# Performance work log

Measured on AMD Instinct MI355X. Metric: run time of the kernel, lower is better.

The kernel has to match this reference:

```python
import jax, jax.numpy as jnp
import numpy as np

# model constants (match init_kwargs)
VOCAB = 32000
DIM = 1024
HEADS = 8
DH = DIM // HEADS
LAYERS = 2
K_SLOTS = 128
KR = 16   # read top-k
KW = 16   # write top-k
CHUNK = 256
GAMMA = 0.9  # slot memory decay per chunk


def setup_inputs() -> dict:
    key = jax.random.key(0)
    ks = jax.random.split(key, 12)
    B, S = 2, 4096
    s = 0.02
    inp = {
        "tokens": jax.random.randint(ks[0], (B, S), 0, VOCAB, dtype=jnp.int32),
        "embed": jax.random.normal(ks[1], (VOCAB, DIM), jnp.float32) * s,
        "Wq": jax.random.normal(ks[2], (LAYERS, DIM, DIM), jnp.float32) * s,
        "Wk": jax.random.normal(ks[3], (LAYERS, DIM, DIM), jnp.float32) * s,
        "Wv": jax.random.normal(ks[4], (LAYERS, DIM, DIM), jnp.float32) * s,
        "Wo": jax.random.normal(ks[5], (LAYERS, DIM, DIM), jnp.float32) * s,
        "slot_keys": jax.random.normal(ks[6], (LAYERS, HEADS, K_SLOTS, DH), jnp.float32) * s,
        "ln_g": jnp.ones((LAYERS, DIM), jnp.float32),
        "ln_b": jnp.zeros((LAYERS, DIM), jnp.float32),
        "fg": jnp.ones((DIM,), jnp.float32),
        "fb": jnp.zeros((DIM,), jnp.float32),
        "Wout": jax.random.normal(ks[7], (DIM, VOCAB), jnp.float32) * s,
        "bout": jnp.zeros((VOCAB,), jnp.float32),
    }
    return inp


def _layer_norm(x, g, b, eps=1e-5):
    mu = jnp.mean(x, axis=-1, keepdims=True)
    var = jnp.var(x, axis=-1, keepdims=True)
    return (x - mu) * jax.lax.rsqrt(var + eps) * g + b


def _mhdsra2_layer(x, M, Wq, Wk, Wv, Wo, sk, causal_mask):
    # x: [B,T,D], M: [B,H,K,dh] slot value memory, sk: [H,K,dh] slot keys
    B, T, D = x.shape
    H, K, dh = sk.shape
    scale = 1.0 / np.sqrt(dh)
    q = (x @ Wq).reshape(B, T, H, dh).transpose(0, 2, 1, 3)  # bhtd
    k = (x @ Wk).reshape(B, T, H, dh).transpose(0, 2, 1, 3)
    v = (x @ Wv).reshape(B, T, H, dh).transpose(0, 2, 1, 3)
    # --- slot READ: top-kr addressed gather from memory ---
    rs = jnp.einsum('bhtd,hkd->bhtk', q, sk) * scale           # [B,H,T,K]
    rv, ri = jax.lax.top_k(rs, KR)                              # [B,H,T,KR]
    rw = jax.nn.softmax(rv, axis=-1)
    gathered = jnp.take_along_axis(M[:, :, None, :, :], ri[..., None], axis=3)  # [B,H,T,KR,dh]
    read = jnp.einsum('bhtk,bhtkd->bhtd', rw, gathered)
    # --- local causal attention within chunk (local_window = chunk_size) ---
    att = jnp.einsum('bhtd,bhsd->bhts', q, k) * scale
    att = jnp.where(causal_mask, att, jnp.float32(-1e9))
    att = jax.nn.softmax(att, axis=-1)
    local = jnp.einsum('bhts,bhsd->bhtd', att, v)
    out = (local + read).transpose(0, 2, 1, 3).reshape(B, T, D) @ Wo
    # --- slot WRITE: top-kw addressed scatter into memory ---
    ws = jnp.einsum('bhtd,hkd->bhtk', k, sk) * scale
    wv_, wi = jax.lax.top_k(ws, KW)
    ww = jax.nn.softmax(wv_, axis=-1)                           # [B,H,T,KW]
    contrib = ww[..., None] * v[:, :, :, None, :]               # [B,H,T,KW,dh]
    bI = jnp.arange(B)[:, None, None, None]
    hI = jnp.arange(H)[None, :, None, None]
    delta = jnp.zeros_like(M).at[bI, hI, wi].add(contrib)
    M_next = GAMMA * M + delta
    return out, M_next


def reference(tokens, embed, Wq, Wk, Wv, Wo, slot_keys, ln_g, ln_b, fg, fb, Wout, bout):
    B, S = tokens.shape
    hidden = embed[tokens]                                      # [B,S,D]
    n_chunks = S // CHUNK
    chunks = hidden.reshape(B, n_chunks, CHUNK, DIM).transpose(1, 0, 2, 3)
    M0 = jnp.zeros((LAYERS, B, HEADS, K_SLOTS, DH), jnp.float32)
    causal_mask = jnp.tril(jnp.ones((CHUNK, CHUNK), bool))

    def body(M_all, chunk):
        new_Ms = []
        for l in range(LAYERS):
            residual = chunk
            xn = _layer_norm(chunk, ln_g[l], ln_b[l])
            out, Mn = _mhdsra2_layer(xn, M_all[l], Wq[l], Wk[l], Wv[l], Wo[l], slot_keys[l], causal_mask)
            new_Ms.append(jax.lax.stop_gradient(Mn))  # detach_state=True
            chunk = residual + out
        return jnp.stack(new_Ms), chunk

    _, outs = jax.lax.scan(body, M0, chunks)                    # [n_chunks,B,T,D]
    out = outs.transpose(1, 0, 2, 3).reshape(B, S, DIM)
    out = _layer_norm(out, fg, fb)
    return out @ Wout + bout                                     # [B,S,VOCAB]
```

## Files before the change

kernel.cpp:

```cpp
#include <hip/hip_runtime.h>

#define DIMM 1024
#define NHEADS 8
#define DH 128
#define NSLOTS 128
#define CHUNK 256
#define NCHUNK 16
#define NB 2
#define SEQ 4096
#define NROWS (NB * SEQ)
#define NVOCAB 32000
#define GAMMA64 0.9
#define SCALE64 0.08838834764831845
#define TAU 1e-6f
#define MAXFLAG 65536

typedef unsigned short u16;
typedef __attribute__((ext_vector_type(4))) float f32x4;
typedef __attribute__((ext_vector_type(8))) short s16x8;

struct alignas(8) u16x4 { u16 x, y, z, w; };

__device__ __forceinline__ u16 f2bf(float f) {
  union { float f; unsigned u; } v; v.f = f;
  return (u16)((v.u + 0x7FFFu + ((v.u >> 16) & 1u)) >> 16);
}
__device__ __forceinline__ float bf2f(u16 u) {
  union { unsigned u; float f; } v; v.u = ((unsigned)u) << 16; return v.f;
}
__device__ __forceinline__ void split3s(float x, u16& h, u16& m, u16& l) {
  h = f2bf(x); float r = x - bf2f(h);
  m = f2bf(r); float r2 = r - bf2f(m);
  l = f2bf(r2);
}

__device__ __forceinline__ void gld16(void* lds, const void* g) {
  __builtin_amdgcn_global_load_lds(
      (const __attribute__((address_space(1))) unsigned*)g,
      (__attribute__((address_space(3))) unsigned*)lds, 16, 0, 0);
}
__device__ __forceinline__ f32x4 mfma16(s16x8 a, s16x8 b, f32x4 c) {
  return __builtin_amdgcn_mfma_f32_16x16x32_bf16(a, b, c, 0, 0, 0);
}

__global__ __launch_bounds__(256) void embed64_kernel(
    const int* __restrict__ tok, const float* __restrict__ emb,
    double* __restrict__ hid) {
  const int row = blockIdx.x;
  const int t = tok[row];
  const float4 v = ((const float4*)(emb + (size_t)t * DIMM))[threadIdx.x];
  double* o = hid + (size_t)row * DIMM + threadIdx.x * 4;
  o[0] = (double)v.x; o[1] = (double)v.y; o[2] = (double)v.z; o[3] = (double)v.w;
}

template <int MODE>
__global__ __launch_bounds__(256) void ln64_kernel(
    const double* __restrict__ x, const float* __restrict__ g,
    const float* __restrict__ bb, double* __restrict__ o64,
    u16* __restrict__ oh, u16* __restrict__ om, u16* __restrict__ ol) {
  const int row = blockIdx.x, tid = threadIdx.x;
  const double* xr = x + (size_t)row * DIMM + tid * 4;
  const double v0 = xr[0], v1 = xr[1], v2 = xr[2], v3 = xr[3];
  __shared__ double red[4];
  double s1 = v0 + v1 + v2 + v3;
#pragma unroll
  for (int off = 32; off >= 1; off >>= 1) s1 += __shfl_xor(s1, off);
  if ((tid & 63) == 0) red[tid >> 6] = s1;
  __syncthreads();
  const double mu = (red[0] + red[1] + red[2] + red[3]) * (1.0 / DIMM);
  __syncthreads();
  const double d0 = v0 - mu, d1 = v1 - mu, d2 = v2 - mu, d3 = v3 - mu;
  double s2 = d0 * d0 + d1 * d1 + d2 * d2 + d3 * d3;
#pragma unroll
  for (int off = 32; off >= 1; off >>= 1) s2 += __shfl_xor(s2, off);
  if ((tid & 63) == 0) red[tid >> 6] = s2;
  __syncthreads();
  const double var = (red[0] + red[1] + red[2] + red[3]) * (1.0 / DIMM);
  const double rs = 1.0 / sqrt(var + 1e-5);
  const float4 g4 = ((const float4*)g)[tid];
  const float4 b4 = ((const float4*)bb)[tid];
  const double y0 = d0 * rs * (double)g4.x + (double)b4.x;
  const double y1 = d1 * rs * (double)g4.y + (double)b4.y;
  const double y2 = d2 * rs * (double)g4.z + (double)b4.z;
  const double y3 = d3 * rs * (double)g4.w + (double)b4.w;
  if (MODE == 0) {
    double* o = o64 + (size_t)row * DIMM + tid * 4;
    o[0] = y0; o[1] = y1; o[2] = y2; o[3] = y3;
    u16x4 rh, rm, rl;
    split3s((float)y0, rh.x, rm.x, rl.x);
    split3s((float)y1, rh.y, rm.y, rl.y);
    split3s((float)y2, rh.z, rm.z, rl.z);
    split3s((float)y3, rh.w, rm.w, rl.w);
    ((u16x4*)(oh + (size_t)row * DIMM))[tid] = rh;
    ((u16x4*)(om + (size_t)row * DIMM))[tid] = rm;
    ((u16x4*)(ol + (size_t)row * DIMM))[tid] = rl;
  } else {
    u16x4 r;
    r.x = f2bf((float)y0); r.y = f2bf((float)y1);
    r.z = f2bf((float)y2); r.w = f2bf((float)y3);
    ((u16x4*)(oh + (size_t)row * DIMM))[tid] = r;
  }
}

__global__ void transconv3_kernel(const float* __restrict__ W,
                                  u16* __restrict__ WTh, u16* __restrict__ WTm,
                                  u16* __restrict__ WTl, int K, int N) {
  __shared__ float tile[32][33];
  const int n0 = blockIdx.x * 32, k0 = blockIdx.y * 32;
  const int tx = threadIdx.x, ty = threadIdx.y;
#pragma unroll
  for (int i = 0; i < 4; i++)
    tile[ty + 8 * i][tx] = W[(size_t)(k0 + ty + 8 * i) * N + n0 + tx];
  __syncthreads();
#pragma unroll
  for (int i = 0; i < 4; i++) {
    u16 h, m, l;
    split3s(tile[tx][ty + 8 * i], h, m, l);
    const size_t o = (size_t)(n0 + ty + 8 * i) * K + k0 + tx;
    WTh[o] = h; WTm[o] = m; WTl[o] = l;
  }
}

__global__ __launch_bounds__(256) void cvt3_32_kernel(
    const float* __restrict__ in, u16* __restrict__ oh, u16* __restrict__ om,
    u16* __restrict__ ol) {
  const size_t i = (size_t)blockIdx.x * 256 + threadIdx.x;
  const float4 v = ((const float4*)in)[i];
  u16x4 rh, rm, rl;
  split3s(v.x, rh.x, rm.x, rl.x); split3s(v.y, rh.y, rm.y, rl.y);
  split3s(v.z, rh.z, rm.z, rl.z); split3s(v.w, rh.w, rm.w, rl.w);
  ((u16x4*)oh)[i] = rh; ((u16x4*)om)[i] = rm; ((u16x4*)ol)[i] = rl;
}

__global__ __launch_bounds__(256) void w2_kernel(const float* __restrict__ W,
                                                 const float* __restrict__ sk,
                                                 double* __restrict__ W2) {
  __shared__ float sksh[128];
  const int r = blockIdx.x, h = r >> 7;
  const int tid = threadIdx.x;
  if (tid < 128) sksh[tid] = sk[(size_t)r * DH + tid];
  __syncthreads();
  for (int d = tid; d < DIMM; d += 256) {
    const float* wrow = W + (size_t)d * DIMM + h * DH;
    double acc = 0.0;
#pragma unroll 8
    for (int j = 0; j < 128; j++) acc += (double)wrow[j] * (double)sksh[j];
    W2[(size_t)r * DIMM + d] = acc;
  }
}

template <bool RES, typename TC>
__global__ __launch_bounds__(256) void gemm3d_kernel(
    const u16* __restrict__ Ah, const u16* __restrict__ Am,
    const u16* __restrict__ Al, const u16* __restrict__ Bh,
    const u16* __restrict__ Bm, const u16* __restrict__ Bl,
    TC* __restrict__ C, const TC* __restrict__ Cres, int M, int N, int K) {
  __shared__ u16 lds[6 * 128 * 32];
  const int tid = threadIdx.x;
  const int bn = blockIdx.x, bm = blockIdx.y;
  const int wid = tid >> 6, lane = tid & 63;
  const int wr = (wid >> 1) * 64, wc = (wid & 1) * 64;
  f32x4 acc[4][4] = {};
  const int row0 = tid >> 2;
  const int colb = (tid & 3) << 4;
  const u16* Gs[6] = {Ah, Am, Al, Bh, Bm, Bl};
  const char* g0[6];
  const char* g1[6];
  char* lb[6];
#pragma unroll
  for (int i = 0; i < 6; i++) {
    const int rbase = (i < 3 ? bm : bn) * 128;
    g0[i] = (const char*)Gs[i] + ((size_t)(rbase + row0) * K) * 2 + colb;
    g1[i] = (const char*)Gs[i] + ((size_t)(rbase + row0 + 64) * K) * 2 + colb;
    lb[i] = (char*)lds + i * 8192 + (tid & 192) * 16;
  }
  const int fo = (lane & 15) * 64 + (lane >> 4) * 16;
  const char* paH = (const char*)lds + 0 + wr * 64 + fo;
  const char* paM = paH + 8192;
  const char* paL = paH + 16384;
  const char* pbH = (const char*)lds + 24576 + wc * 64 + fo;
  const char* pbM = pbH + 8192;
  const char* pbL = pbH + 16384;

  for (int k0 = 0; k0 < K; k0 += 32) {
    const size_t kb = (size_t)k0 * 2;
#pragma unroll
    for (int i = 0; i < 6; i++) {
      gld16(lb[i], g0[i] + kb);
      gld16(lb[i] + 4096, g1[i] + kb);
    }
    __syncthreads();
    s16x8 bh[4], bm_[4], bl[4];
#pragma unroll
    for (int n = 0; n < 4; n++) {
      bh[n] = *(const s16x8*)(pbH + n * 1024);
      bm_[n] = *(const s16x8*)(pbM + n * 1024);
      bl[n] = *(const s16x8*)(pbL + n * 1024);
    }
#pragma unroll
    for (int m = 0; m < 4; m++) {
      const s16x8 ah = *(const s16x8*)(paH + m * 1024);
      const s16x8 am = *(const s16x8*)(paM + m * 1024);
      const s16x8 al = *(const s16x8*)(paL + m * 1024);
#pragma unroll
      for (int n = 0; n < 4; n++) {
        f32x4 t = acc[m][n];
        t = mfma16(al, bh[n], t);
        t = mfma16(ah, bl[n], t);
        t = mfma16(am, bm_[n], t);
        t = mfma16(am, bh[n], t);
        t = mfma16(ah, bm_[n], t);
        t = mfma16(ah, bh[n], t);
        acc[m][n] = t;
      }
    }
    __syncthreads();
  }
#pragma unroll
  for (int m = 0; m < 4; m++)
#pragma unroll
    for (int n = 0; n < 4; n++)
#pragma unroll
      for (int j = 0; j < 4; j++) {
        const int r = bm * 128 + wr + m * 16 + (lane >> 4) * 4 + j;
        const int c = bn * 128 + wc + n * 16 + (lane & 15);
        TC v = (TC)acc[m][n][j];
        if (RES) v += Cres[(size_t)r * N + c];
        C[(size_t)r * N + c] = v;
      }
}

__global__ __launch_bounds__(256) void score3_kernel(
    const u16* __restrict__ Qh, const u16* __restrict__ Qm,
    const u16* __restrict__ Ql, const u16* __restrict__ Kh3,
    const u16* __restrict__ Km3, const u16* __restrict__ Kl3,
    const u16* __restrict__ skh, const u16* __restrict__ skm,
    const u16* __restrict__ skl, float* __restrict__ S) {
  __shared__ u16 lds[6 * 128 * 32];
  const int tid = threadIdx.x;
  const int bm = blockIdx.x;
  const int y = blockIdx.y;
  const int which = y >> 4, b = (y >> 3) & 1, h = y & 7;
  const u16* Ah = which ? Kh3 : Qh;
  const u16* Am = which ? Km3 : Qm;
  const u16* Al = which ? Kl3 : Ql;
  const int wid = tid >> 6, lane = tid & 63;
  const int wr = (wid >> 1) * 64, wc = (wid & 1) * 64;
  f32x4 acc[4][4] = {};
  const int row0 = tid >> 2;
  const int colb = (tid & 3) << 4;
  const size_t arow = (size_t)(b * SEQ + bm * 128);
  const u16* Gs[6] = {Ah, Am, Al, skh, skm, skl};
  const char* g0[6];
  const char* g1[6];
  char* lb[6];
#pragma unroll
  for (int i = 0; i < 6; i++) {
    if (i < 3) {
      g0[i] = (const char*)Gs[i] + (arow + row0) * 2048 + h * 256 + colb;
      g1[i] = (const char*)Gs[i] + (arow + row0 + 64) * 2048 + h * 256 + colb;
    } else {
      g0[i] = (const char*)Gs[i] + ((size_t)h * 128 + row0) * 256 + colb;
      g1[i] = (const char*)Gs[i] + ((size_t)h * 128 + row0 + 64) * 256 + colb;
    }
    lb[i] = (char*)lds + i * 8192 + (tid & 192) * 16;
  }
  const int fo = (lane & 15) * 64 + (lane >> 4) * 16;
  const char* paH = (const char*)lds + 0 + wr * 64 + fo;
  const char* paM = paH + 8192;
  const char* paL = paH + 16384;
  const char* pbH = (const char*)lds + 24576 + wc * 64 + fo;
  const char* pbM = pbH + 8192;
  const char* pbL = pbH + 16384;

  for (int k0 = 0; k0 < DH; k0 += 32) {
    const size_t kb = (size_t)k0 * 2;
#pragma unroll
    for (int i = 0; i < 6; i++) {
      gld16(lb[i], g0[i] + kb);
      gld16(lb[i] + 4096, g1[i] + kb);
    }
    __syncthreads();
    s16x8 bh[4], bm_[4], bl[4];
#pragma unroll
    for (int n = 0; n < 4; n++) {
      bh[n] = *(const s16x8*)(pbH + n * 1024);
      bm_[n] = *(const s16x8*)(pbM + n * 1024);
      bl[n] = *(const s16x8*)(pbL + n * 1024);
    }
#pragma unroll
    for (int m = 0; m < 4; m++) {
      const s16x8 ah = *(const s16x8*)(paH + m * 1024);
      const s16x8 am = *(const s16x8*)(paM + m * 1024);
      const s16x8 al = *(const s16x8*)(paL + m * 1024);
#pragma unroll
      for (int n = 0; n < 4; n++) {
        f32x4 t = acc[m][n];
        t = mfma16(al, bh[n], t);
        t = mfma16(ah, bl[n], t);
        t = mfma16(am, bm_[n], t);
        t = mfma16(am, bh[n], t);
        t = mfma16(ah, bm_[n], t);
        t = mfma16(ah, bh[n], t);
        acc[m][n] = t;
      }
    }
    __syncthreads();
  }
  const size_t sbase =
      (size_t)which * 65536 + (size_t)(b * 8 + h) * 4096 + (size_t)bm * 128;
#pragma unroll
  for (int m = 0; m < 4; m++)
#pragma unroll
    for (int n = 0; n < 4; n++)
#pragma unroll
      for (int j = 0; j < 4; j++) {
        const int r = wr + m * 16 + (lane >> 4) * 4 + j;
        const int c = wc + n * 16 + (lane & 15);
        S[(sbase + r) * NSLOTS + c] = acc[m][n][j];
      }
}

__global__ __launch_bounds__(256) void select_kernel(
    const float* __restrict__ S, int* __restrict__ riQ, int* __restrict__ riK,
    double* __restrict__ rwQ, double* __restrict__ rwK,
    int* __restrict__ fcnts, int* __restrict__ flq, int* __restrict__ flk) {
  const int which = blockIdx.y;
  int* oidx = which ? riK : riQ;
  double* ow = which ? rwK : rwQ;
  int* fcnt = fcnts + which;
  int* flist = which ? flk : flq;
  const int wid = threadIdx.x >> 6, lane = threadIdx.x & 63;
  const int rid = blockIdx.x * 4 + wid;
  const float2 sv =
      *(const float2*)(S + ((size_t)which * 65536 + rid) * NSLOTS + lane * 2);
  const float sc = (float)SCALE64;
  float v0 = sv.x * sc, v1 = sv.y * sc;
  const int i0 = lane * 2, i1 = lane * 2 + 1;
  float selv = -1e30f; int seli = 0;
  for (int it = 0; it < 17; it++) {
    float m; int mi;
    if (v1 > v0) { m = v1; mi = i1; } else { m = v0; mi = i0; }
#pragma unroll
    for (int off = 1; off < 64; off <<= 1) {
      const float om = __shfl_xor(m, off);
      const int oi = __shfl_xor(mi, off);
      if (om > m || (om == m && oi < mi)) { m = om; mi = oi; }
    }
    if (lane == it) { selv = m; seli = mi; }
    if (mi == i0) v0 = -1e30f;
    if (mi == i1) v1 = -1e30f;
  }
  const float mx = __shfl(selv, 0);
  const float v15 = __shfl(selv, 15);
  const float v16 = __shfl(selv, 16);
  if (lane == 0 && (v15 - v16) < TAU) {
    const int p = atomicAdd(fcnt, 1);
    if (p < MAXFLAG) flist[p] = rid;
  }
  const float e = (lane < 16) ? expf(selv - mx) : 0.0f;
  double ss = (double)e;
  ss += __shfl_xor(ss, 1); ss += __shfl_xor(ss, 2);
  ss += __shfl_xor(ss, 4); ss += __shfl_xor(ss, 8);
  if (lane < 16) {
    ow[(size_t)rid * 16 + lane] = (double)e / ss;
    oidx[(size_t)rid * 16 + lane] = seli;
  }
}

__global__ __launch_bounds__(256) void fixup_kernel(
    const int* __restrict__ fcnts, const int* __restrict__ flq,
    const int* __restrict__ flk, const double* __restrict__ xn,
    const double* __restrict__ W2q, const double* __restrict__ W2k,
    int* __restrict__ riQ, int* __restrict__ riK, double* __restrict__ rwQ,
    double* __restrict__ rwK) {
  __shared__ double xsh[1024];
  __shared__ double psh[256];
  __shared__ double ssh[128];
  const int which = blockIdx.y;
  const int* flist = which ? flk : flq;
  const double* W2 = which ? W2k : W2q;
  int* oidx = which ? riK : riQ;
  double* ow = which ? rwK : rwQ;
  const int tid = threadIdx.x;
  const int n = min(fcnts[which], MAXFLAG);
  for (int i = blockIdx.x; i < n; i += gridDim.x) {
    __syncthreads();
    const int rid = flist[i];
    const int t = rid & 4095, h = (rid >> 12) & 7, b = rid >> 15;
    const double* xr = xn + ((size_t)b * SEQ + t) * DIMM;
    for (int j = tid; j < DIMM; j += 256) xsh[j] = xr[j];
    __syncthreads();
    const int slot = tid >> 1, half = tid & 1;
    const double* w2r = W2 + (size_t)(h * NSLOTS + slot) * DIMM + half * 512;
    const double* xp = xsh + half * 512;
    double acc = 0.0;
#pragma unroll 8
    for (int d = 0; d < 512; d++) acc += xp[d] * w2r[d];
    psh[tid] = acc;
    __syncthreads();
    if (tid < 128) ssh[tid] = (psh[2 * tid] + psh[2 * tid + 1]) * SCALE64;
    __syncthreads();
    if (tid < 64) {
      const int lane = tid;
      double selv = -1e300; int seli = 0;
      double v0 = ssh[lane], v1 = ssh[lane + 64];
      for (int it = 0; it < 16; it++) {
        double m; int mi;
        if (v1 > v0) { m = v1; mi = lane + 64; } else { m = v0; mi = lane; }
#pragma unroll
        for (int off = 1; off < 64; off <<= 1) {
          const double om = __shfl_xor(m, off);
          const int oi = __shfl_xor(mi, off);
          if (om > m || (om == m && oi < mi)) { m = om; mi = oi; }
        }
        if (lane == it) { selv = m; seli = mi; }
        if (mi == lane) v0 = -1e300;
        if (mi == lane + 64) v1 = -1e300;
      }
      const double mx = __shfl(selv, 0);
      const float e = (lane < 16) ? expf((float)(selv - mx)) : 0.0f;
      double ss = (double)e;
      ss += __shfl_xor(ss, 1); ss += __shfl_xor(ss, 2);
      ss += __shfl_xor(ss, 4); ss += __shfl_xor(ss, 8);
      if (lane < 16) {
        ow[(size_t)rid * 16 + lane] = (double)e / ss;
        oidx[(size_t)rid * 16 + lane] = seli;
      }
    }
  }
}

__global__ __launch_bounds__(512) void delta64_kernel(
    const int* __restrict__ wi, const double* __restrict__ ww,
    const float* __restrict__ V, double* __restrict__ delta) {
  __shared__ short slot_sh[4096];
  __shared__ double w_sh[4096];
  __shared__ u16 list[4096];
  __shared__ int cnt[NSLOTS], off_[NSLOTS];
  const int bid = blockIdx.x;
  const int c = bid & 15, h = (bid >> 4) & 7, b = bid >> 7;
  const int tid = threadIdx.x;
  if (tid < NSLOTS) cnt[tid] = 0;
  __syncthreads();
  const size_t ebase = ((size_t)(b * 8 + h) * SEQ + (size_t)c * CHUNK) * 16;
#pragma unroll
  for (int i = 0; i < 8; i++) {
    const int e = tid + i * 512;
    const int s = wi[ebase + e];
    slot_sh[e] = (short)s;
    w_sh[e] = ww[ebase + e];
    atomicAdd(&cnt[s], 1);
  }
  __syncthreads();
  if (tid == 0) {
    int a = 0;
    for (int s = 0; s < NSLOTS; s++) { off_[s] = a; a += cnt[s]; }
  }
  __syncthreads();
  if (tid < NSLOTS) {
    int p = off_[tid];
    const short me = (short)tid;
    for (int e = 0; e < 4096; e++)
      if (slot_sh[e] == me) list[p++] = (u16)e;
  }
  __syncthreads();
  const int slot = tid >> 2, dbase = (tid & 3) * 32;
  double acc[32] = {};
  const int start = off_[slot], len = cnt[slot];
  const float* vbase =
      V + ((size_t)b * SEQ + (size_t)c * CHUNK) * DIMM + h * DH + dbase;
  for (int i = 0; i < len; i++) {
    const int e = list[start + i];
    const double w = w_sh[e];
    const float* vp = vbase + (size_t)(e >> 4) * DIMM;
#pragma unroll
    for (int d = 0; d < 32; d++) acc[d] += w * (double)vp[d];
  }
  double* dst = delta + ((size_t)bid * NSLOTS + slot) * DH + dbase;
#pragma unroll
  for (int d = 0; d < 32; d++) dst[d] = acc[d];
}

__global__ __launch_bounds__(256) void attn_fused(
    const float* __restrict__ Q, const float* __restrict__ Kb,
    const float* __restrict__ V, float* __restrict__ outb) {
  __shared__ float Qs[32][130];
  __shared__ float KVs[16][130];
  const int idx = blockIdx.x;
  const int rq = idx & 7, h = (idx >> 3) & 7, c = (idx >> 6) & 15, b = idx >> 10;
  const int tid = threadIdx.x;
  const size_t rowbase = (size_t)b * SEQ + (size_t)c * CHUNK;
  {
    const int r = tid >> 3, d0 = (tid & 7) * 16;
    const float* qp = Q + (rowbase + rq * 32 + r) * DIMM + h * DH + d0;
#pragma unroll
    for (int j = 0; j < 16; j++) Qs[r][d0 + j] = qp[j];
  }
  const int row = tid >> 3;
  const int sub = tid & 7;
  const int row_abs = rq * 32 + row;
  const int ntile = 2 * rq + 2;
  float pexp[16][2];
#pragma unroll
  for (int kt = 0; kt < 16; kt++) { pexp[kt][0] = -1e30f; pexp[kt][1] = -1e30f; }

#pragma unroll
  for (int kt = 0; kt < 16; kt++) {
    if (kt < ntile) {
      __syncthreads();
      {
        const int r = tid >> 4, d0 = (tid & 15) * 8;
        const float* kp = Kb + (rowbase + kt * 16 + r) * DIMM + h * DH + d0;
#pragma unroll
        for (int j = 0; j < 8; j++) KVs[r][d0 + j] = kp[j];
      }
      __syncthreads();
#pragma unroll
      for (int kk = 0; kk < 2; kk++) {
        const int key = sub * 2 + kk;
        double s = 0.0;
#pragma unroll 8
        for (int d = 0; d < DH; d++)
          s += (double)Qs[row][d] * (double)KVs[key][d];
        const int kabs = kt * 16 + key;
        pexp[kt][kk] = (kabs <= row_abs) ? (float)(s * SCALE64) : -1e30f;
      }
    }
  }
  float m = -1e30f;
#pragma unroll
  for (int kt = 0; kt < 16; kt++) {
    m = fmaxf(m, pexp[kt][0]); m = fmaxf(m, pexp[kt][1]);
  }
  m = fmaxf(m, __shfl_xor(m, 1));
  m = fmaxf(m, __shfl_xor(m, 2));
  m = fmaxf(m, __shfl_xor(m, 4));
  double ss = 0.0;
#pragma unroll
  for (int kt = 0; kt < 16; kt++) {
#pragma unroll
    for (int j = 0; j < 2; j++) {
      const float e = __expf(pexp[kt][j] - m);
      pexp[kt][j] = e;
      ss += (double)e;
    }
  }
  ss += __shfl_xor(ss, 1); ss += __shfl_xor(ss, 2); ss += __shfl_xor(ss, 4);
  const double inv = 1.0 / ss;
#pragma unroll
  for (int kt = 0; kt < 16; kt++) {
    pexp[kt][0] = (float)((double)pexp[kt][0] * inv);
    pexp[kt][1] = (float)((double)pexp[kt][1] * inv);
  }
  double acc[16] = {};
#pragma unroll
  for (int kt = 0; kt < 16; kt++) {
    if (kt < ntile) {
      __syncthreads();
      {
        const int r = tid >> 4, d0 = (tid & 15) * 8;
        const float* vp = V + (rowbase + kt * 16 + r) * DIMM + h * DH + d0;
#pragma unroll
        for (int j = 0; j < 8; j++) KVs[r][d0 + j] = vp[j];
      }
      __syncthreads();
#pragma unroll
      for (int key = 0; key < 16; key++) {
        const int src = (tid & 56) | (key >> 1);
        const float pf = __shfl(pexp[kt][key & 1], src, 64);
        const double pd = (double)pf;
        const float* vr = &KVs[key][sub * 16];
#pragma unroll
        for (int d = 0; d < 16; d++) acc[d] += pd * (double)vr[d];
      }
    }
  }
  float* op = outb + (rowbase + row_abs) * DIMM + h * DH + sub * 16;
#pragma unroll
  for (int d = 0; d < 16; d++) op[d] = (float)acc[d];
}

__global__ __launch_bounds__(256) void recur64_kernel(
    const int* __restrict__ ri, const double* __restrict__ rw,
    const double* __restrict__ delta, const float* __restrict__ inb,
    u16* __restrict__ sh, u16* __restrict__ sm, u16* __restrict__ sl) {
  __shared__ double Msh[NSLOTS][17];
  const int bid = blockIdx.x;
  const int ds = bid & 7, h = (bid >> 3) & 7, b = bid >> 6;
  const int tid = threadIdx.x;
  for (int i = tid; i < NSLOTS * 17; i += 256) ((double*)Msh)[i] = 0.0;
  __syncthreads();
  for (int c = 0; c < NCHUNK; c++) {
    const size_t rbase =
        ((size_t)(b * 8 + h) * SEQ + (size_t)c * CHUNK + tid) * 16;
    double a[16] = {};
#pragma unroll
    for (int j = 0; j < 16; j++) {
      const int slot = ri[rbase + j];
      const double w = rw[rbase + j];
      const double* mp = &Msh[slot][0];
#pragma unroll
      for (int d = 0; d < 16; d++) a[d] += w * mp[d];
    }
    const size_t base = ((size_t)b * SEQ + (size_t)c * CHUNK + tid) * DIMM +
                        h * DH + ds * 16;
    const float* ip = inb + base;
    u16x4 rh[4], rm[4], rl[4];
#pragma unroll
    for (int q = 0; q < 4; q++) {
      float f0 = (float)((double)ip[q * 4 + 0] + a[q * 4 + 0]);
      float f1 = (float)((double)ip[q * 4 + 1] + a[q * 4 + 1]);
      float f2 = (float)((double)ip[q * 4 + 2] + a[q * 4 + 2]);
      float f3 = (float)((double)ip[q * 4 + 3] + a[q * 4 + 3]);
      split3s(f0, rh[q].x, rm[q].x, rl[q].x);
      split3s(f1, rh[q].y, rm[q].y, rl[q].y);
      split3s(f2, rh[q].z, rm[q].z, rl[q].z);
      split3s(f3, rh[q].w, rm[q].w, rl[q].w);
    }
#pragma unroll
    for (int q = 0; q < 4; q++) {
      ((u16x4*)(sh + base))[q] = rh[q];
      ((u16x4*)(sm + base))[q] = rm[q];
      ((u16x4*)(sl + base))[q] = rl[q];
    }
    __syncthreads();
    const int slot = tid >> 1, d8 = (tid & 1) * 8;
    const double* dp = delta +
        (((size_t)(b * 8 + h) * NCHUNK + c) * NSLOTS + slot) * DH + ds * 16 + d8;
#pragma unroll
    for (int d = 0; d < 8; d++)
      Msh[slot][d8 + d] = GAMMA64 * Msh[slot][d8 + d] + dp[d];
    __syncthreads();
  }
}

__global__ void transconv_kernel(const float* __restrict__ W,
                                 u16* __restrict__ WT, int K, int N) {
  __shared__ float tile[32][33];
  const int n0 = blockIdx.x * 32, k0 = blockIdx.y * 32;
  const int tx = threadIdx.x, ty = threadIdx.y;
#pragma unroll
  for (int i = 0; i < 4; i++)
    tile[ty + 8 * i][tx] = W[(size_t)(k0 + ty + 8 * i) * N + n0 + tx];
  __syncthreads();
#pragma unroll
  for (int i = 0; i < 4; i++)
    WT[(size_t)(n0 + ty + 8 * i) * K + k0 + tx] = f2bf(tile[tx][ty + 8 * i]);
}

template <bool BIAS>
__global__ __launch_bounds__(256) void gemm_kernel(
    const u16* __restrict__ A, const u16* __restrict__ B, float* __restrict__ C,
    const float* __restrict__ bias, int M, int N, int K) {
  __shared__ u16 As[128 * 32];
  __shared__ u16 Bs[128 * 32];
  const int tid = threadIdx.x;
  const int lid = blockIdx.y * gridDim.x + blockIdx.x;
  const int npm = M / 128;
  const int ngrid = N / 128;
  const int GN = 16;
  const int ppg = GN * npm;
  const int gid = lid / ppg;
  const int first_n = gid * GN;
  const int gsz = min(GN, ngrid - first_n);
  const int local = lid - gid * ppg;
  const int bn = first_n + local % gsz;
  const int bm = local / gsz;
  const int wid = tid >> 6, lane = tid & 63;
  const int wr = (wid >> 1) * 64, wc = (wid & 1) * 64;
  f32x4 acc[4][4] = {};
  const int row0 = tid >> 2;
  const int colb = (tid & 3) << 4;
  const char* A0 = (const char*)A + ((size_t)(bm * 128 + row0) * K) * 2 + colb;
  const char* A1 = (const char*)A + ((size_t)(bm * 128 + row0 + 64) * K) * 2 + colb;
  const char* B0 = (const char*)B + ((size_t)(bn * 128 + row0) * K) * 2 + colb;
  const char* B1 = (const char*)B + ((size_t)(bn * 128 + row0 + 64) * K) * 2 + colb;
  char* lA0 = (char*)As + (tid & 192) * 16;
  char* lB0 = (char*)Bs + (tid & 192) * 16;
  const char* pa = (const char*)As + wr * 64 + (lane & 15) * 64 + (lane >> 4) * 16;
  const char* pb = (const char*)Bs + wc * 64 + (lane & 15) * 64 + (lane >> 4) * 16;
  for (int k0 = 0; k0 < K; k0 += 32) {
    const size_t kb = (size_t)k0 * 2;
    gld16(lA0, A0 + kb);
    gld16(lA0 + 4096, A1 + kb);
    gld16(lB0, B0 + kb);
    gld16(lB0 + 4096, B1 + kb);
    __syncthreads();
    s16x8 af[4], bf[4];
#pragma unroll
    for (int m = 0; m < 4; m++) af[m] = *(const s16x8*)(pa + m * 1024);
#pragma unroll
    for (int n = 0; n < 4; n++) bf[n] = *(const s16x8*)(pb + n * 1024);
#pragma unroll
    for (int m = 0; m < 4; m++)
#pragma unroll
      for (int n = 0; n < 4; n++) acc[m][n] = mfma16(af[m], bf[n], acc[m][n]);
    __syncthreads();
  }
#pragma unroll
  for (int m = 0; m < 4; m++)
#pragma unroll
    for (int n = 0; n < 4; n++)
#pragma unroll
      for (int j = 0; j < 4; j++) {
        const int r = bm * 128 + wr + m * 16 + (lane >> 4) * 4 + j;
        const int c = bn * 128 + wc + n * 16 + (lane & 15);
        float v = acc[m][n][j];
        if (BIAS) v += bias[c];
        C[(size_t)r * N + c] = v;
      }
}

extern "C" void kernel_launch(void* const* d_in, const int* in_sizes, int n_in,
                              void* d_out, int out_size, void* d_ws,
                              size_t ws_size, hipStream_t stream) {
  (void)in_sizes; (void)n_in; (void)out_size; (void)ws_size;
  const int* tokens = (const int*)d_in[0];
  const float* embed = (const float*)d_in[1];
  const float* Wq = (const float*)d_in[2];
  const float* Wk = (const float*)d_in[3];
  const float* Wv = (const float*)d_in[4];
  const float* Wo = (const float*)d_in[5];
  const float* slot_keys = (const float*)d_in[6];
  const float* ln_g = (const float*)d_in[7];
  const float* ln_b = (const float*)d_in[8];
  const float* fg = (const float*)d_in[9];
  const float* fb = (const float*)d_in[10];
  const float* Wout = (const float*)d_in[11];
  const float* bout = (const float*)d_in[12];
  float* out = (float*)d_out;

  char* p = (char*)d_ws;
  auto alloc = [&](size_t bytes) -> char* {
    char* r = p;
    p += (bytes + 255) & ~(size_t)255;
    return r;
  };
  const size_t RD = (size_t)NROWS * DIMM;
  double* hidden64 = (double*)alloc(RD * 8);
  double* xn64 = (double*)alloc(RD * 8);
  float* q32 = (float*)alloc(RD * 4);
  float* k32 = (float*)alloc(RD * 4);
  float* v32 = (float*)alloc(RD * 4);
  float* local32 = (float*)alloc(RD * 4);
  double* delta64 =
      (double*)alloc((size_t)NB * NHEADS * NCHUNK * NSLOTS * DH * 8);
  int* ri = (int*)alloc((size_t)65536 * 16 * 4);
  int* wi = (int*)alloc((size_t)65536 * 16 * 4);
  double* rw64 = (double*)alloc((size_t)65536 * 16 * 8);
  double* ww64 = (double*)alloc((size_t)65536 * 16 * 8);
  u16* sAh = (u16*)alloc(RD * 2);
  u16* sAm = (u16*)alloc(RD * 2);
  u16* sAl = (u16*)alloc(RD * 2);
  u16* kBh = (u16*)alloc(RD * 2);
  u16* kBm = (u16*)alloc(RD * 2);
  u16* kBl = (u16*)alloc(RD * 2);
  u16* WTh = (u16*)alloc((size_t)8 * DIMM * DIMM * 2);
  u16* WTm = (u16*)alloc((size_t)8 * DIMM * DIMM * 2);
  u16* WTl = (u16*)alloc((size_t)8 * DIMM * DIMM * 2);
  double* W2q = (double*)alloc((size_t)2 * DIMM * DIMM * 8);
  double* W2k = (double*)alloc((size_t)2 * DIMM * DIMM * 8);
  const size_t SKE = (size_t)2 * NHEADS * NSLOTS * DH;
  u16* sk3h = (u16*)alloc(SKE * 2);
  u16* sk3m = (u16*)alloc(SKE * 2);
  u16* sk3l = (u16*)alloc(SKE * 2);
  float* S = (float*)alloc((size_t)2 * 65536 * NSLOTS * 4);
  int* fcnts = (int*)alloc(256);
  int* flq = (int*)alloc((size_t)MAXFLAG * 4);
  int* flk = (int*)alloc((size_t)MAXFLAG * 4);

  u16* xnb = (u16*)q32;
  u16* WoutT = (u16*)k32;

  const float* Wmats[4] = {Wq, Wk, Wv, Wo};
  for (int l = 0; l < 2; l++) {
    for (int w = 0; w < 4; w++) {
      const size_t o = ((size_t)l * 4 + w) * DIMM * DIMM;
      transconv3_kernel<<<dim3(DIMM / 32, DIMM / 32), dim3(32, 8), 0, stream>>>(
          Wmats[w] + (size_t)l * DIMM * DIMM, WTh + o, WTm + o, WTl + o, DIMM,
          DIMM);
    }
    const float* skl = slot_keys + (size_t)l * NHEADS * NSLOTS * DH;
    w2_kernel<<<1024, 256, 0, stream>>>(Wq + (size_t)l * DIMM * DIMM, skl,
                                        W2q + (size_t)l * DIMM * DIMM);
    w2_kernel<<<1024, 256, 0, stream>>>(Wk + (size_t)l * DIMM * DIMM, skl,
                                        W2k + (size_t)l * DIMM * DIMM);
  }
  cvt3_32_kernel<<<SKE / 1024, 256, 0, stream>>>(slot_keys, sk3h, sk3m, sk3l);

  embed64_kernel<<<NROWS, 256, 0, stream>>>(tokens, embed, hidden64);

  const dim3 g3(DIMM / 128, NROWS / 128);
  for (int l = 0; l < 2; l++) {
    const size_t oq = ((size_t)l * 4 + 0) * DIMM * DIMM;
    const size_t ok = ((size_t)l * 4 + 1) * DIMM * DIMM;
    const size_t ov = ((size_t)l * 4 + 2) * DIMM * DIMM;
    const size_t oo = ((size_t)l * 4 + 3) * DIMM * DIMM;
    const size_t sko = (size_t)l * NHEADS * NSLOTS * DH;
    ln64_kernel<0><<<NROWS, 256, 0, stream>>>(hidden64, ln_g + l * DIMM,
                                              ln_b + l * DIMM, xn64, sAh, sAm,
                                              sAl);
    gemm3d_kernel<false, float><<<g3, 256, 0, stream>>>(
        sAh, sAm, sAl, WTh + oq, WTm + oq, WTl + oq, q32, nullptr, NROWS, DIMM,
        DIMM);
    gemm3d_kernel<false, float><<<g3, 256, 0, stream>>>(
        sAh, sAm, sAl, WTh + ok, WTm + ok, WTl + ok, k32, nullptr, NROWS, DIMM,
        DIMM);
    gemm3d_kernel<false, float><<<g3, 256, 0, stream>>>(
        sAh, sAm, sAl, WTh + ov, WTm + ov, WTl + ov, v32, nullptr, NROWS, DIMM,
        DIMM);
    cvt3_32_kernel<<<RD / 1024, 256, 0, stream>>>(q32, sAh, sAm, sAl);
    cvt3_32_kernel<<<RD / 1024, 256, 0, stream>>>(k32, kBh, kBm, kBl);
    hipMemsetAsync(fcnts, 0, 8, stream);
    score3_kernel<<<dim3(32, 32), 256, 0, stream>>>(
        sAh, sAm, sAl, kBh, kBm, kBl, sk3h + sko, sk3m + sko, sk3l + sko, S);
    select_kernel<<<dim3(16384, 2), 256, 0, stream>>>(S, ri, wi, rw64, ww64,
                                                      fcnts, flq, flk);
    fixup_kernel<<<dim3(512, 2), 256, 0, stream>>>(
        fcnts, flq, flk, xn64, W2q + (size_t)l * DIMM * DIMM,
        W2k + (size_t)l * DIMM * DIMM, ri, wi, rw64, ww64);
    delta64_kernel<<<NB * NHEADS * NCHUNK, 512, 0, stream>>>(wi, ww64, v32,
                                                             delta64);
    attn_fused<<<NB * NCHUNK * NHEADS * 8, 256, 0, stream>>>(q32, k32, v32,
                                                             local32);
    recur64_kernel<<<NB * NHEADS * 8, 256, 0, stream>>>(ri, rw64, delta64,
                                                        local32, sAh, sAm,
                                                        sAl);
    gemm3d_kernel<true, double><<<g3, 256, 0, stream>>>(
        sAh, sAm, sAl, WTh + oo, WTm + oo, WTl + oo, hidden64, hidden64, NROWS,
        DIMM, DIMM);
  }
  transconv_kernel<<<dim3(NVOCAB / 32, DIMM / 32), dim3(32, 8), 0, stream>>>(
      Wout, WoutT, DIMM, NVOCAB);
  ln64_kernel<1><<<NROWS, 256, 0, stream>>>(hidden64, fg, fb, nullptr, xnb,
                                            nullptr, nullptr);
  gemm_kernel<true><<<dim3(NVOCAB / 128, NROWS / 128), 256, 0, stream>>>(
      xnb, WoutT, out, bout, NROWS, NVOCAB, DIMM);
}
```

Measured before the change: 5.222 ms.

## Double-buffer output GEMM with 256x128 tiles and split attention dot-product accumulators

The final vocab projection GEMM now uses 512-thread blocks covering 256x128 tiles, double-buffered LDS, and async global-to-LDS loads issued two k-steps ahead, with explicit vmcnt waits. The goal is to overlap memory loads with MFMA work and raise data reuse per block. Separately, the fp64 attention score dot product is split into four independent accumulators to break the serial dependency chain. The cost is higher LDS use and register pressure per block. The four-way split also changes the fp64 summation order slightly.

Measured after the change: 5.371 ms. 1.03x slower.

```diff
diff --git a/kernel.cpp b/kernel.cpp
--- a/kernel.cpp
+++ b/kernel.cpp
@@ -519,10 +519,15 @@
 #pragma unroll
       for (int kk = 0; kk < 2; kk++) {
         const int key = sub * 2 + kk;
-        double s = 0.0;
+        double sa = 0.0, sb = 0.0, sc2 = 0.0, sd = 0.0;
 #pragma unroll 8
-        for (int d = 0; d < DH; d++)
-          s += (double)Qs[row][d] * (double)KVs[key][d];
+        for (int d = 0; d < 32; d++) {
+          sa += (double)Qs[row][d] * (double)KVs[key][d];
+          sb += (double)Qs[row][d + 32] * (double)KVs[key][d + 32];
+          sc2 += (double)Qs[row][d + 64] * (double)KVs[key][d + 64];
+          sd += (double)Qs[row][d + 96] * (double)KVs[key][d + 96];
+        }
+        const double s = (sa + sb) + (sc2 + sd);
         const int kabs = kt * 16 + key;
         pexp[kt][kk] = (kabs <= row_abs) ? (float)(s * SCALE64) : -1e30f;
       }
@@ -649,15 +654,14 @@
     WT[(size_t)(n0 + ty + 8 * i) * K + k0 + tx] = f2bf(tile[tx][ty + 8 * i]);
 }
 
-template <bool BIAS>
-__global__ __launch_bounds__(256) void gemm_kernel(
+__global__ __launch_bounds__(512) void gemm256_kernel(
     const u16* __restrict__ A, const u16* __restrict__ B, float* __restrict__ C,
     const float* __restrict__ bias, int M, int N, int K) {
-  __shared__ u16 As[128 * 32];
-  __shared__ u16 Bs[128 * 32];
+  __shared__ u16 Ab[2][256 * 32];
+  __shared__ u16 Bb[2][128 * 32];
   const int tid = threadIdx.x;
   const int lid = blockIdx.y * gridDim.x + blockIdx.x;
-  const int npm = M / 128;
+  const int npm = M / 256;
   const int ngrid = N / 128;
   const int GN = 16;
   const int ppg = GN * npm;
@@ -667,27 +671,37 @@
   const int local = lid - gid * ppg;
   const int bn = first_n + local % gsz;
   const int bm = local / gsz;
-  const int wid = tid >> 6, lane = tid & 63;
-  const int wr = (wid >> 1) * 64, wc = (wid & 1) * 64;
+  const int w = tid >> 6, lane = tid & 63;
+  const int wm = w >> 1, wn = w & 1;
   f32x4 acc[4][4] = {};
-  const int row0 = tid >> 2;
-  const int colb = (tid & 3) << 4;
-  const char* A0 = (const char*)A + ((size_t)(bm * 128 + row0) * K) * 2 + colb;
-  const char* A1 = (const char*)A + ((size_t)(bm * 128 + row0 + 64) * K) * 2 + colb;
-  const char* B0 = (const char*)B + ((size_t)(bn * 128 + row0) * K) * 2 + colb;
-  const char* B1 = (const char*)B + ((size_t)(bn * 128 + row0 + 64) * K) * 2 + colb;
-  char* lA0 = (char*)As + (tid & 192) * 16;
-  char* lB0 = (char*)Bs + (tid & 192) * 16;
-  const char* pa = (const char*)As + wr * 64 + (lane & 15) * 64 + (lane >> 4) * 16;
-  const char* pb = (const char*)Bs + wc * 64 + (lane & 15) * 64 + (lane >> 4) * 16;
-  for (int k0 = 0; k0 < K; k0 += 32) {
-    const size_t kb = (size_t)k0 * 2;
-    gld16(lA0, A0 + kb);
-    gld16(lA0 + 4096, A1 + kb);
-    gld16(lB0, B0 + kb);
-    gld16(lB0 + 4096, B1 + kb);
-    __syncthreads();
+  const int srow = tid >> 2;
+  const int scolb = (tid & 3) << 4;
+  const char* Ag0 = (const char*)A + ((size_t)(bm * 256 + srow) * K) * 2 + scolb;
+  const char* Ag1 =
+      (const char*)A + ((size_t)(bm * 256 + 128 + srow) * K) * 2 + scolb;
+  const char* Bg = (const char*)B + ((size_t)(bn * 128 + srow) * K) * 2 + scolb;
+  const int wbase = (tid & 448) * 16;
+  const int aoff = (wm * 64 + (lane & 15)) * 64 + (lane >> 4) * 16;
+  const int boff = (wn * 64 + (lane & 15)) * 64 + (lane >> 4) * 16;
+  const int NT = K / 32;
+
+  gld16((char*)Ab[0] + wbase, Ag0);
+  gld16((char*)Ab[0] + 8192 + wbase, Ag1);
+  gld16((char*)Bb[0] + wbase, Bg);
+  gld16((char*)Ab[1] + wbase, Ag0 + 64);
+  gld16((char*)Ab[1] + 8192 + wbase, Ag1 + 64);
+  gld16((char*)Bb[1] + wbase, Bg + 64);
+
+  for (int t = 0; t < NT; t++) {
+    const int p = t & 1;
+    if (t == NT - 1)
+      asm volatile("s_waitcnt vmcnt(0)" ::: "memory");
+    else
+      asm volatile("s_waitcnt vmcnt(3)" ::: "memory");
+    __builtin_amdgcn_s_barrier();
     s16x8 af[4], bf[4];
+    const char* pa = (const char*)Ab[p] + aoff;
+    const char* pb = (const char*)Bb[p] + boff;
 #pragma unroll
     for (int m = 0; m < 4; m++) af[m] = *(const s16x8*)(pa + m * 1024);
 #pragma unroll
@@ -696,7 +710,14 @@
     for (int m = 0; m < 4; m++)
 #pragma unroll
       for (int n = 0; n < 4; n++) acc[m][n] = mfma16(af[m], bf[n], acc[m][n]);
-    __syncthreads();
+    __builtin_amdgcn_s_barrier();
+    __builtin_amdgcn_sched_barrier(0);
+    if (t + 2 < NT) {
+      const size_t kb = (size_t)(t + 2) * 64;
+      gld16((char*)Ab[p] + wbase, Ag0 + kb);
+      gld16((char*)Ab[p] + 8192 + wbase, Ag1 + kb);
+      gld16((char*)Bb[p] + wbase, Bg + kb);
+    }
   }
 #pragma unroll
   for (int m = 0; m < 4; m++)
@@ -704,11 +725,9 @@
     for (int n = 0; n < 4; n++)
 #pragma unroll
       for (int j = 0; j < 4; j++) {
-        const int r = bm * 128 + wr + m * 16 + (lane >> 4) * 4 + j;
-        const int c = bn * 128 + wc + n * 16 + (lane & 15);
-        float v = acc[m][n][j];
-        if (BIAS) v += bias[c];
-        C[(size_t)r * N + c] = v;
+        const int r = bm * 256 + wm * 64 + m * 16 + (lane >> 4) * 4 + j;
+        const int c = bn * 128 + wn * 64 + n * 16 + (lane & 15);
+        C[(size_t)r * N + c] = acc[m][n][j] + bias[c];
       }
 }
 
@@ -835,6 +854,6 @@
       Wout, WoutT, DIMM, NVOCAB);
   ln64_kernel<1><<<NROWS, 256, 0, stream>>>(hidden64, fg, fb, nullptr, xnb,
                                             nullptr, nullptr);
-  gemm_kernel<true><<<dim3(NVOCAB / 128, NROWS / 128), 256, 0, stream>>>(
+  gemm256_kernel<<<dim3(NVOCAB / 128, NROWS / 256), 512, 0, stream>>>(
       xnb, WoutT, out, bout, NROWS, NVOCAB, DIMM);
 }
```
